# Performance work log

Hardware: AMD Instinct MI355X
Metric: run time of the kernel (lower is better)

Reference implementation:

```python
import jax, jax.numpy as jnp
import numpy as np

NUM_CLASSES = 19
K = 100                 # max_views_per_class
TEMP = 0.1
BASE_TEMP = 0.07
EPS_NORM = 1e-12


def _l2_normalize(x):
    # matches torch F.normalize(dim=1): x / max(||x||, eps)
    n = jnp.sqrt(jnp.sum(x * x, axis=1, keepdims=True))
    return x / jnp.maximum(n, EPS_NORM)


def _sample_indices(labels_flat):
    # Deterministic per-class sampler: first K pixels of each class.
    # (torch version uses randperm; the downstream math is identical.)
    # Every class is guaranteed >= K pixels by input construction.
    idxs = [jnp.where(labels_flat == c, size=K, fill_value=0)[0]
            for c in range(NUM_CLASSES)]
    return jnp.concatenate(idxs)  # [NUM_CLASSES*K]


def setup_inputs() -> dict:
    key = jax.random.key(0)
    k1, k2, k3, k4 = jax.random.split(key, 4)
    pixel_feats = jax.random.normal(k1, (8, 256, 128, 128), dtype=jnp.float32)
    labels = jax.random.randint(k2, (8, 128, 128), 0, NUM_CLASSES).astype(jnp.int64)
    memory_feats = jax.random.normal(k3, (20000, 256), dtype=jnp.float32)
    memory_labels = jax.random.randint(k4, (20000,), 0, NUM_CLASSES).astype(jnp.int64)
    return {"pixel_feats": pixel_feats, "labels": labels,
            "memory_feats": memory_feats, "memory_labels": memory_labels}


def reference(pixel_feats, labels, memory_feats, memory_labels):
    B, D, H, W = pixel_feats.shape
    feats_flat = pixel_feats.transpose(0, 2, 3, 1).reshape(-1, D)   # [B*H*W, D]
    labels_flat = labels.reshape(-1)

    idx = _sample_indices(labels_flat)
    anchor_feats = feats_flat[idx]                                  # [Na, D]
    anchor_labels = jnp.repeat(jnp.arange(NUM_CLASSES), K)          # [Na]

    contrast_feats = jnp.concatenate([anchor_feats, memory_feats], axis=0)
    contrast_labels = jnp.concatenate([anchor_labels, memory_labels], axis=0)

    a = _l2_normalize(anchor_feats)
    c = _l2_normalize(contrast_feats)
    logits = jnp.einsum('nd,md->nm', a, c) / TEMP                   # [Na, Nc]

    Na, Nc = logits.shape
    mask = (anchor_labels[:, None] == contrast_labels[None, :]).astype(logits.dtype)
    # remove self-contrast (diagonal of the first Na contrast columns)
    rows = jnp.arange(Na)
    logits_mask = jnp.ones((Na, Nc), dtype=logits.dtype).at[rows, rows].set(0.0)
    mask = mask * logits_mask

    exp_logits = jnp.exp(logits) * logits_mask
    log_prob = logits - jnp.log(exp_logits.sum(axis=1, keepdims=True) + 1e-12)

    pos_count = mask.sum(axis=1)                                    # [Na]
    valid = pos_count > 0
    mean_log_prob_pos = (mask * log_prob).sum(axis=1) / jnp.maximum(pos_count, 1.0)
    n_valid = jnp.maximum(jnp.sum(valid).astype(logits.dtype), 1.0)
    loss = -(TEMP / BASE_TEMP) * (jnp.sum(jnp.where(valid, mean_log_prob_pos, 0.0)) / n_valid)
    return loss
```

## Files before the change

### kernel.cpp

```cpp
#include <hip/hip_runtime.h>
#include <hip/hip_bf16.h>
#include <math.h>

#define NCLS   19
#define KPC    100
#define NA     1900
#define NM     20000
#define NC     21900
#define NCP2   22016
#define D      256
#define HW     16384
#define NPIX   131072
#define NT_M   15
#define NT_N   172
#define NTILES (NT_M * NT_N)

#define ABPC    13
#define B_ANCH  0
#define B_MEM   247
#define B_CLAB  2747
#define B_PAD   2833
#define B_ZERO  2848
#define K1_GRID 2849

typedef __attribute__((ext_vector_type(8))) short bf16x8;
typedef __attribute__((ext_vector_type(4))) float f32x4;

#define WS_ROWS  64
#define WS_ROWP  7744
#define WS_CLAB  30720
#define WS_CT2   118784

__device__ __forceinline__ short f2bf(float x) {
    __hip_bfloat16 h = __float2bfloat16(x);
    return *(short*)&h;
}

__global__ void prep_kernel(const float* __restrict__ pixel, const int* __restrict__ labels,
                            const float* __restrict__ mem, const int* __restrict__ memlab,
                            int* __restrict__ clab, short* __restrict__ Ct2,
                            float* __restrict__ rowS, float* __restrict__ rowP) {
    const int b = blockIdx.x;
    const int t = threadIdx.x;
    if (b < B_MEM) {
        const int c    = b / ABPC;
        const int r0   = (b % ABPC) * 8;
        const int rmax = (r0 + 8 < KPC) ? r0 + 8 : KPC;
        const int wave = t >> 6, lane = t & 63;
        __shared__ int s_idx[8];
        __shared__ int s_base;
        __shared__ int s_wavecnt[4];
        if (t == 0) s_base = 0;
        __syncthreads();
        for (int start = 0; start < NPIX; start += 256) {
            const int i = start + t;
            const bool pred = (labels[i] == c);
            const unsigned long long bm = __ballot(pred);
            if (lane == 0) s_wavecnt[wave] = __popcll(bm);
            __syncthreads();
            const int base = s_base;
            int wbase = 0;
            for (int w = 0; w < wave; ++w) wbase += s_wavecnt[w];
            const int chunk_total = s_wavecnt[0] + s_wavecnt[1] + s_wavecnt[2] + s_wavecnt[3];
            if (pred) {
                const int rank = base + wbase + __popcll(bm & ((1ULL << lane) - 1ULL));
                if (rank >= r0 && rank < rmax) s_idx[rank - r0] = i;
            }
            __syncthreads();
            if (t == 0) s_base = base + chunk_total;
            if (base + chunk_total >= rmax) break;
        }
        __syncthreads();
        const int ai = t >> 5;
        const int kq = t & 31;
        const int r  = r0 + ai;
        if (r < rmax) {
            const int a   = c * KPC + r;
            const int pix = s_idx[ai];
            const int bi  = pix >> 14;
            const int hw  = pix & (HW - 1);
            const float* base = pixel + ((size_t)(bi * D + kq * 8)) * HW + hw;
            float v[8];
            float ssq = 0.f;
            #pragma unroll
            for (int j = 0; j < 8; ++j) { v[j] = base[(size_t)j * HW]; ssq += v[j] * v[j]; }
            #pragma unroll
            for (int o = 16; o; o >>= 1) ssq += __shfl_xor(ssq, o, 32);
            const float inv = 1.0f / fmaxf(sqrtf(ssq), 1e-12f);
            bf16x8 ov;
            #pragma unroll
            for (int j = 0; j < 8; ++j) ov[j] = f2bf(v[j] * inv);
            *(bf16x8*)(Ct2 + ((size_t)kq * NCP2 + a) * 8) = ov;
        }
    } else if (b < B_CLAB) {
        const int r  = (b - B_MEM) * 8 + (t >> 5);
        const int kq = t & 31;
        const float4 v0 = *(const float4*)(mem + (size_t)r * D + kq * 8);
        const float4 v1 = *(const float4*)(mem + (size_t)r * D + kq * 8 + 4);
        float ssq = v0.x*v0.x + v0.y*v0.y + v0.z*v0.z + v0.w*v0.w
                  + v1.x*v1.x + v1.y*v1.y + v1.z*v1.z + v1.w*v1.w;
        #pragma unroll
        for (int o = 16; o; o >>= 1) ssq += __shfl_xor(ssq, o, 32);
        const float inv = 1.0f / fmaxf(sqrtf(ssq), 1e-12f);
        bf16x8 ov;
        ov[0] = f2bf(v0.x * inv); ov[1] = f2bf(v0.y * inv);
        ov[2] = f2bf(v0.z * inv); ov[3] = f2bf(v0.w * inv);
        ov[4] = f2bf(v1.x * inv); ov[5] = f2bf(v1.y * inv);
        ov[6] = f2bf(v1.z * inv); ov[7] = f2bf(v1.w * inv);
        *(bf16x8*)(Ct2 + ((size_t)kq * NCP2 + NA + r) * 8) = ov;
    } else if (b < B_PAD) {
        const int i = (b - B_CLAB) * 256 + t;
        clab[i] = (i < NA) ? ((i * 5243) >> 19)
                           : ((i < NC) ? memlab[i - NA] : -1);
    } else if (b < B_ZERO) {
        const int e = (b - B_PAD) * 256 + t;
        if (e < 32 * (NCP2 - NC)) {
            const int kq = e / (NCP2 - NC);
            const int n  = NC + (e - kq * (NCP2 - NC));
            bf16x8 z = {};
            *(bf16x8*)(Ct2 + ((size_t)kq * NCP2 + n) * 8) = z;
        }
    } else {
        for (int i = t; i < 1920; i += 256) { rowS[i] = 0.f; rowP[i] = 0.f; }
    }
}

__global__ __launch_bounds__(256, 4)
void mfma_gemm_kernel(const short* __restrict__ Ct2, const int* __restrict__ clab,
                      float* __restrict__ rowS, float* __restrict__ rowP) {
    __shared__ int s_nlab[128];
    const int tid  = threadIdx.x;
    const int lane = tid & 63;
    const int w    = tid >> 6;
    const int wm   = w >> 1, wn = w & 1;
    const int quad = lane >> 4;
    const int l16  = lane & 15;

    const int bid = blockIdx.x;
    const int x   = bid & 7;
    const int j   = bid >> 3;
    const int wg  = (x < 4 ? x * 323 : 1292 + (x - 4) * 322) + j;
    const int m0  = (wg % NT_M) * 128;
    const int n0  = (wg / NT_M) * 128;

    if (tid < 128) s_nlab[tid] = clab[n0 + tid];

    const int aCol = m0 + wm * 64 + l16;
    const int bCol = n0 + wn * 64 + l16;

    f32x4 acc[4][4] = {};

    #pragma unroll
    for (int kb = 0; kb < 8; ++kb) {
        const int kqb = kb * 4 + quad;
        const short* kbase = Ct2 + (size_t)kqb * NCP2 * 8;
        bf16x8 af[4], bfr[4];
        #pragma unroll
        for (int mi = 0; mi < 4; ++mi)
            af[mi] = *(const bf16x8*)(kbase + (size_t)(aCol + mi * 16) * 8);
        #pragma unroll
        for (int ni = 0; ni < 4; ++ni)
            bfr[ni] = *(const bf16x8*)(kbase + (size_t)(bCol + ni * 16) * 8);
        #pragma unroll
        for (int ni = 0; ni < 4; ++ni)
            #pragma unroll
            for (int mi = 0; mi < 4; ++mi)
                acc[ni][mi] = __builtin_amdgcn_mfma_f32_16x16x32_bf16(
                    bfr[ni], af[mi], acc[ni][mi], 0, 0, 0);
    }

    __syncthreads();

    const int m_base = m0 + wm * 64 + l16;
    #pragma unroll
    for (int mi = 0; mi < 4; ++mi) {
        const int m    = m_base + mi * 16;
        const int mlab = (m * 5243) >> 19;
        float s = 0.f, p = 0.f;
        #pragma unroll
        for (int ni = 0; ni < 4; ++ni) {
            const int nb = wn * 64 + ni * 16 + quad * 4;
            const int4 lb = *(const int4*)&s_nlab[nb];
            #pragma unroll
            for (int r = 0; r < 4; ++r) {
                const int n  = n0 + nb + r;
                const int nl = (&lb.x)[r];
                if (n < NC && n != m) {
                    const float l = acc[ni][mi][r] * 10.0f;
                    s += __expf(l);
                    if (nl == mlab) p += l;
                }
            }
        }
        s += __shfl_xor(s, 16, 64); s += __shfl_xor(s, 32, 64);
        p += __shfl_xor(p, 16, 64); p += __shfl_xor(p, 32, 64);
        if (quad == 0 && m < NA) {
            atomicAdd(&rowS[m], s);
            atomicAdd(&rowP[m], p);
        }
    }
}

__global__ void finalize_kernel(const float* __restrict__ rowS, const float* __restrict__ rowP,
                                const int* __restrict__ memlab, float* __restrict__ out) {
    const int t = threadIdx.x;
    __shared__ int hist[NCLS];
    __shared__ float rs[4], rn[4];
    if (t < NCLS) hist[t] = 0;
    __syncthreads();
    for (int i4 = t; i4 < NM / 4; i4 += 256) {
        const int4 v = ((const int4*)memlab)[i4];
        atomicAdd(&hist[v.x], 1);
        atomicAdd(&hist[v.y], 1);
        atomicAdd(&hist[v.z], 1);
        atomicAdd(&hist[v.w], 1);
    }
    __syncthreads();
    float sum = 0.f, nval = 0.f;
    for (int n = t; n < NA; n += 256) {
        const float cnt  = (float)(KPC - 1 + hist[(n * 5243) >> 19]);
        const float logS = logf(rowS[n] + 1e-12f);
        const float mean = (rowP[n] - cnt * logS) / fmaxf(cnt, 1.0f);
        if (cnt > 0.f) { sum += mean; nval += 1.f; }
    }
    for (int o = 32; o; o >>= 1) {
        sum  += __shfl_xor(sum, o, 64);
        nval += __shfl_xor(nval, o, 64);
    }
    if ((t & 63) == 0) { rs[t >> 6] = sum; rn[t >> 6] = nval; }
    __syncthreads();
    if (t == 0) {
        const float s  = rs[0] + rs[1] + rs[2] + rs[3];
        const float nv = rn[0] + rn[1] + rn[2] + rn[3];
        out[0] = -(0.1f / 0.07f) * (s / fmaxf(nv, 1.f));
    }
}

extern "C" void kernel_launch(void* const* d_in, const int* in_sizes, int n_in,
                              void* d_out, int out_size, void* d_ws, size_t ws_size,
                              hipStream_t stream) {
    const float* pixel  = (const float*)d_in[0];
    const int*   labels = (const int*)d_in[1];
    const float* mem    = (const float*)d_in[2];
    const int*   memlab = (const int*)d_in[3];
    char* ws = (char*)d_ws;
    float* rowS = (float*)(ws + WS_ROWS);
    float* rowP = (float*)(ws + WS_ROWP);
    int*   clab = (int*)(ws + WS_CLAB);
    short* Ct2  = (short*)(ws + WS_CT2);
    float* out  = (float*)d_out;

    prep_kernel<<<dim3(K1_GRID), dim3(256), 0, stream>>>(
        pixel, labels, mem, memlab, clab, Ct2, rowS, rowP);
    mfma_gemm_kernel<<<dim3(NTILES), dim3(256), 0, stream>>>(Ct2, clab, rowS, rowP);
    finalize_kernel<<<dim3(1), dim3(256), 0, stream>>>(rowS, rowP, memlab, out);
}
```

Before: 230.4 us.

## Stage GEMM operand tiles in LDS via direct global-to-LDS loads

The GEMM kernel used to have every wave load its A and B fragments straight from global memory. It now stages each 128x64 K-chunk of A and B into shared memory with global_load_lds, then reads the MFMA fragments from LDS in two sub-steps per chunk. The aim is to cut redundant global and L2 traffic, since waves sharing rows or columns used to fetch the same data separately. The price is two barriers per chunk with no double buffering, so loads are not overlapped with compute. Occupancy drops from the launch bound of 4 blocks to 3, and 32 KB of LDS is now used per block.

```diff
diff --git a/kernel.cpp b/kernel.cpp
--- a/kernel.cpp
+++ b/kernel.cpp
@@ -125,9 +125,11 @@
     }
 }
 
-__global__ __launch_bounds__(256, 4)
+__global__ __launch_bounds__(256, 3)
 void mfma_gemm_kernel(const short* __restrict__ Ct2, const int* __restrict__ clab,
                       float* __restrict__ rowS, float* __restrict__ rowP) {
+    __shared__ __align__(16) short As[8 * 128 * 8];
+    __shared__ __align__(16) short Bs[8 * 128 * 8];
     __shared__ int s_nlab[128];
     const int tid  = threadIdx.x;
     const int lane = tid & 63;
@@ -145,31 +147,45 @@
 
     if (tid < 128) s_nlab[tid] = clab[n0 + tid];
 
-    const int aCol = m0 + wm * 64 + l16;
-    const int bCol = n0 + wn * 64 + l16;
-
     f32x4 acc[4][4] = {};
 
-    #pragma unroll
-    for (int kb = 0; kb < 8; ++kb) {
-        const int kqb = kb * 4 + quad;
-        const short* kbase = Ct2 + (size_t)kqb * NCP2 * 8;
-        bf16x8 af[4], bfr[4];
-        #pragma unroll
-        for (int mi = 0; mi < 4; ++mi)
-            af[mi] = *(const bf16x8*)(kbase + (size_t)(aCol + mi * 16) * 8);
-        #pragma unroll
-        for (int ni = 0; ni < 4; ++ni)
-            bfr[ni] = *(const bf16x8*)(kbase + (size_t)(bCol + ni * 16) * 8);
-        #pragma unroll
-        for (int ni = 0; ni < 4; ++ni)
+    for (int kc = 0; kc < 4; ++kc) {
+        #pragma unroll
+        for (int i = 0; i < 4; ++i) {
+            const int bl = (w * 4 + i) * 64;
+            const int kq = bl >> 7;
+            const int ml = bl & 127;
+            const size_t gA = ((size_t)(kc * 8 + kq) * NCP2 + m0 + ml + lane) * 8;
+            __builtin_amdgcn_global_load_lds(
+                (const __attribute__((address_space(1))) void*)(Ct2 + gA),
+                (__attribute__((address_space(3))) void*)(As + (size_t)bl * 8 + lane * 8),
+                16, 0, 0);
+            const size_t gB = ((size_t)(kc * 8 + kq) * NCP2 + n0 + ml + lane) * 8;
+            __builtin_amdgcn_global_load_lds(
+                (const __attribute__((address_space(1))) void*)(Ct2 + gB),
+                (__attribute__((address_space(3))) void*)(Bs + (size_t)bl * 8 + lane * 8),
+                16, 0, 0);
+        }
+        __syncthreads();
+        #pragma unroll
+        for (int ks = 0; ks < 2; ++ks) {
+            const int kqb = ks * 4 + quad;
+            bf16x8 af[4], bfr[4];
             #pragma unroll
             for (int mi = 0; mi < 4; ++mi)
-                acc[ni][mi] = __builtin_amdgcn_mfma_f32_16x16x32_bf16(
-                    bfr[ni], af[mi], acc[ni][mi], 0, 0, 0);
-    }
-
-    __syncthreads();
+                af[mi] = *(const bf16x8*)(As + ((kqb * 128) + wm * 64 + mi * 16 + l16) * 8);
+            #pragma unroll
+            for (int ni = 0; ni < 4; ++ni)
+                bfr[ni] = *(const bf16x8*)(Bs + ((kqb * 128) + wn * 64 + ni * 16 + l16) * 8);
+            #pragma unroll
+            for (int ni = 0; ni < 4; ++ni)
+                #pragma unroll
+                for (int mi = 0; mi < 4; ++mi)
+                    acc[ni][mi] = __builtin_amdgcn_mfma_f32_16x16x32_bf16(
+                        bfr[ni], af[mi], acc[ni][mi], 0, 0, 0);
+        }
+        __syncthreads();
+    }
 
     const int m_base = m0 + wm * 64 + l16;
     #pragma unroll
```

New measurement: 224.6 us. 2.5% less time.
